# Kernel tuning notes

Hardware: AMD Instinct MI355X
Metric: run time of the kernel (lower is better)

Reference implementation:

```python
import jax, jax.numpy as jnp
import numpy as np

S, D, H, MLP = 2048, 1024, 16, 4096
DK = D // H
EPS = 1e-5  # torch LayerNorm default


def setup_inputs() -> dict:
    key = jax.random.key(0)
    ks = jax.random.split(key, 8)
    init = lambda k, shape, fan_in: jax.random.normal(k, shape, jnp.float32) * (fan_in ** -0.5)
    return {
        "x": jax.random.normal(ks[0], (S, D), jnp.float32),
        "wq": init(ks[1], (D, D), D), "bq": jnp.zeros((D,), jnp.float32),
        "wk": init(ks[2], (D, D), D), "bk": jnp.zeros((D,), jnp.float32),
        "wv": init(ks[3], (D, D), D), "bv": jnp.zeros((D,), jnp.float32),
        "wo": init(ks[4], (D, D), D), "bo": jnp.zeros((D,), jnp.float32),
        "w1": init(ks[5], (D, MLP), D), "b1": jnp.zeros((MLP,), jnp.float32),
        "w2": init(ks[6], (MLP, D), MLP), "b2": jnp.zeros((D,), jnp.float32),
        "ln1_g": jnp.ones((D,), jnp.float32), "ln1_b": jnp.zeros((D,), jnp.float32),
        "ln2_g": jnp.ones((D,), jnp.float32), "ln2_b": jnp.zeros((D,), jnp.float32),
    }


def _layernorm(x, g, b):
    m = jnp.mean(x, axis=-1, keepdims=True)
    v = jnp.var(x, axis=-1, keepdims=True)
    return (x - m) * jax.lax.rsqrt(v + EPS) * g + b


def reference(x, wq, bq, wk, bk, wv, bv, wo, bo, w1, b1, w2, b2, ln1_g, ln1_b, ln2_g, ln2_b):
    # --- residual 1: pre-LN multi-head self-attention ---
    h = _layernorm(x, ln1_g, ln1_b)
    q = (h @ wq + bq).reshape(S, H, DK).transpose(1, 0, 2)  # [H,S,DK]
    k = (h @ wk + bk).reshape(S, H, DK).transpose(1, 0, 2)
    v = (h @ wv + bv).reshape(S, H, DK).transpose(1, 0, 2)
    scores = jnp.einsum('hqd,hkd->hqk', q, k) / jnp.sqrt(jnp.float32(DK))  # [H,S,S]
    attn = jax.nn.softmax(scores, axis=-1)
    o = jnp.einsum('hqk,hkd->hqd', attn, v)  # [H,S,DK]
    # Faithful to original: x.contiguous().view(S, -1) is a raw reshape of the
    # [H,S,DK] buffer (no transpose back to [S,H,DK]).
    o = o.reshape(S, D)
    x = x + (o @ wo + bo)
    # --- residual 2: pre-LN GELU FFN ---
    h2 = _layernorm(x, ln2_g, ln2_b)
    f = jax.nn.gelu(h2 @ w1 + b1, approximate=False)  # torch nn.GELU = exact erf
    x = x + (f @ w2 + b2)
    return x
```

## Files before the change

### kernel.cpp

```cpp
#include <hip/hip_runtime.h>


constexpr int kS = 2048, kD = 1024, kH = 16, kDK = 64, kMLP = 4096;
constexpr float kEps = 1e-5f;

using u16 = unsigned short;
using u32 = unsigned int;
typedef float f32x4 __attribute__((ext_vector_type(4)));
typedef short bf16x8 __attribute__((ext_vector_type(8)));

__device__ __forceinline__ u16 f2b(float f) {
  u32 u = __builtin_bit_cast(u32, f);
  return (u16)((u + 0x7fffu + ((u >> 16) & 1u)) >> 16);
}

typedef const __attribute__((address_space(1))) u32* gas1;
typedef __attribute__((address_space(3))) u32* las3;
__device__ __forceinline__ void async16(const void* g, void* l) {
  __builtin_amdgcn_global_load_lds((gas1)g, (las3)l, 16, 0, 0);
}

__global__ __launch_bounds__(256)
void ln_kernel(const float* __restrict__ x, const float* __restrict__ g,
               const float* __restrict__ b, u16* __restrict__ out) {
  __shared__ float red[8];
  const int row = blockIdx.x, tid = threadIdx.x;
  const float4 v = *(const float4*)(x + (size_t)row * kD + tid * 4);
  float s = v.x + v.y + v.z + v.w;
  float ss = v.x * v.x + v.y * v.y + v.z * v.z + v.w * v.w;
#pragma unroll
  for (int d = 1; d < 64; d <<= 1) { s += __shfl_xor(s, d); ss += __shfl_xor(ss, d); }
  if ((tid & 63) == 0) { red[tid >> 6] = s; red[4 + (tid >> 6)] = ss; }
  __syncthreads();
  const float m = (red[0] + red[1] + red[2] + red[3]) * (1.f / kD);
  const float var = (red[4] + red[5] + red[6] + red[7]) * (1.f / kD) - m * m;
  const float r = rsqrtf(var + kEps);
  const float4 gv = *(const float4*)(g + tid * 4);
  const float4 bv = *(const float4*)(b + tid * 4);
  ushort4 o;
  o.x = f2b((v.x - m) * r * gv.x + bv.x);
  o.y = f2b((v.y - m) * r * gv.y + bv.y);
  o.z = f2b((v.z - m) * r * gv.z + bv.z);
  o.w = f2b((v.w - m) * r * gv.w + bv.w);
  *(ushort4*)(out + (size_t)row * kD + tid * 4) = o;
}

__global__ __launch_bounds__(256)
void transpose_cvt(const float* __restrict__ in, u16* __restrict__ out, int R, int C) {
  __shared__ float tile[32][33];
  const int c0 = blockIdx.x * 32, r0 = blockIdx.y * 32;
  const int x = threadIdx.x, y = threadIdx.y;
#pragma unroll
  for (int i = 0; i < 4; ++i)
    tile[y + i * 8][x] = in[(size_t)(r0 + y + i * 8) * C + c0 + x];
  __syncthreads();
#pragma unroll
  for (int i = 0; i < 4; ++i)
    out[(size_t)(c0 + y + i * 8) * R + r0 + x] = f2b(tile[x][y + i * 8]);
}

__global__ void concat_bias(const float* __restrict__ bq, const float* __restrict__ bk,
                            const float* __restrict__ bv, float* __restrict__ out) {
  int i = blockIdx.x * 256 + threadIdx.x;
  out[i] = i < kD ? bq[i] : (i < 2 * kD ? bk[i - kD] : bv[i - 2 * kD]);
}

__global__ __launch_bounds__(256)
void vtrans(const u16* __restrict__ qkv, u16* __restrict__ vt) {
  __shared__ u16 t[64][72];
  const int s0 = blockIdx.x * 64, h = blockIdx.y, tid = threadIdx.x;
#pragma unroll
  for (int r = 0; r < 2; ++r) {
    int chunk = r * 256 + tid, row = chunk >> 3, col = (chunk & 7) * 8;
    uint4 v = *(const uint4*)(qkv + (size_t)(s0 + row) * 3072 + 2 * kD + h * 64 + col);
    *(uint4*)(&t[row][col]) = v;
  }
  __syncthreads();
#pragma unroll
  for (int r = 0; r < 2; ++r) {
    int chunk = r * 256 + tid, drow = chunk >> 3, scol = (chunk & 7) * 8;
    u16 tmp[8];
#pragma unroll
    for (int j = 0; j < 8; ++j) tmp[j] = t[scol + j][drow];
    *(uint4*)(vt + (size_t)h * 64 * kS + (size_t)drow * kS + s0 + scol) = *(uint4*)tmp;
  }
}

template <int EPI>
__global__ __launch_bounds__(256, 2)
void gemm_bt(const u16* __restrict__ A, const u16* __restrict__ Bt,
             const float* __restrict__ bias, void* __restrict__ Cout,
             int N, int K, int Ksub) {
  constexpr int BM = 128, BN = 128, BK = 32;
  constexpr int MT = 4, NT = 4;
  __shared__ u16 As[BM * BK];
  __shared__ u16 Bs[BN * BK];
  const int tid = threadIdx.x;
  const int w = tid >> 6, l = tid & 63;
  const int wm = w >> 1, wn = w & 1;
  const int row0 = blockIdx.y * BM, col0 = blockIdx.x * BN;
  const int koff = blockIdx.z * Ksub;

  const int sc = ((l & 3) ^ ((l >> 3) & 3)) * 8;
  const u16* Ag = A + (size_t)(row0 + w * 16 + (l >> 2)) * K + koff + sc;
  const u16* Bg = Bt + (size_t)(col0 + w * 16 + (l >> 2)) * K + koff + sc;
  u16* AsW = As + w * 512;
  u16* BsW = Bs + w * 512;

  f32x4 acc[MT][NT] = {};
  const int q = l >> 4;

  for (int kt = 0; kt < Ksub; kt += BK) {
#pragma unroll
    for (int r = 0; r < 2; ++r) async16(Ag + (size_t)r * 64 * K + kt, AsW + r * 2048);
#pragma unroll
    for (int r = 0; r < 2; ++r) async16(Bg + (size_t)r * 64 * K + kt, BsW + r * 2048);
    __syncthreads();
    bf16x8 af[MT], bfr[NT];
#pragma unroll
    for (int i = 0; i < MT; ++i) {
      const int ra = wm * 64 + i * 16 + (l & 15);
      af[i] = *(const bf16x8*)(As + ra * 32 + (q ^ ((ra >> 1) & 3)) * 8);
    }
#pragma unroll
    for (int j = 0; j < NT; ++j) {
      const int rb = wn * 64 + j * 16 + (l & 15);
      bfr[j] = *(const bf16x8*)(Bs + rb * 32 + (q ^ ((rb >> 1) & 3)) * 8);
    }
#pragma unroll
    for (int i = 0; i < MT; ++i)
#pragma unroll
      for (int j = 0; j < NT; ++j)
        acc[i][j] = __builtin_amdgcn_mfma_f32_16x16x32_bf16(af[i], bfr[j], acc[i][j], 0, 0, 0);
    __syncthreads();
  }

  float* Pf = nullptr;
  if constexpr (EPI == 3)
    Pf = (float*)Cout + (size_t)blockIdx.z * gridDim.y * BM * N;
#pragma unroll
  for (int i = 0; i < MT; ++i) {
    const int row = row0 + wm * 64 + i * 16 + ((l >> 4) << 2);
#pragma unroll
    for (int j = 0; j < NT; ++j) {
      const int col = col0 + wn * 64 + j * 16 + (l & 15);
      float bb = 0.f;
      if constexpr (EPI != 3) bb = bias[col];
#pragma unroll
      for (int r = 0; r < 4; ++r) {
        const size_t idx = (size_t)(row + r) * N + col;
        float v = acc[i][j][r] + bb;
        if constexpr (EPI == 0) {
          ((u16*)Cout)[idx] = f2b(v);
        } else if constexpr (EPI == 1) {
          ((u16*)Cout)[idx] = f2b(0.5f * v * (1.f + erff(v * 0.7071067811865475f)));
        } else {
          Pf[idx] = v;
        }
      }
    }
  }
}

template <int KS>
__global__ __launch_bounds__(256)
void reduce_add(const float* __restrict__ parts, const float* __restrict__ bias,
                const float* __restrict__ res, float* __restrict__ out,
                int N, size_t strideMN) {
  const size_t b = ((size_t)blockIdx.x * 256 + threadIdx.x) * 4;
  float4 a = *(const float4*)(res + b);
  const float4 bv = *(const float4*)(bias + (b & (size_t)(N - 1)));
  a.x += bv.x; a.y += bv.y; a.z += bv.z; a.w += bv.w;
#pragma unroll
  for (int s = 0; s < KS; ++s) {
    const float4 p = *(const float4*)(parts + s * strideMN + b);
    a.x += p.x; a.y += p.y; a.z += p.z; a.w += p.w;
  }
  *(float4*)(out + b) = a;
}

__global__ __launch_bounds__(256, 2)
void flash_attn(const u16* __restrict__ qkv, const u16* __restrict__ vt,
                u16* __restrict__ og) {
  constexpr int LQ = 72;
  constexpr int LV = 136;
  __shared__ u16 Qs[64 * LQ];
  __shared__ u16 Ks[128 * LQ];
  __shared__ u16 Vs[64 * LV];
  __shared__ u16 Ps[4][16 * LV];
  const int tid = threadIdx.x, w = tid >> 6, l = tid & 63;
  const int h = blockIdx.y, q0 = blockIdx.x * 64;

#pragma unroll
  for (int r = 0; r < 2; ++r) {
    int chunk = r * 256 + tid, row = chunk >> 3, col = (chunk & 7) * 8;
    uint4 v = *(const uint4*)(qkv + (size_t)(q0 + row) * 3072 + h * 64 + col);
    *(uint4*)(&Qs[row * LQ + col]) = v;
  }
  __syncthreads();
  bf16x8 qa[2];
#pragma unroll
  for (int kq = 0; kq < 2; ++kq)
    qa[kq] = *(const bf16x8*)(&Qs[(w * 16 + (l & 15)) * LQ + kq * 32 + (l >> 4) * 8]);

  f32x4 oacc[4] = {};
  float mi[4], li[4];
#pragma unroll
  for (int r = 0; r < 4; ++r) { mi[r] = -1e30f; li[r] = 0.f; }

  for (int kt = 0; kt < kS; kt += 128) {
    __syncthreads();
#pragma unroll
    for (int r = 0; r < 4; ++r) {
      int chunk = r * 256 + tid, row = chunk >> 3, col = (chunk & 7) * 8;
      uint4 v = *(const uint4*)(qkv + (size_t)(kt + row) * 3072 + kD + h * 64 + col);
      *(uint4*)(&Ks[row * LQ + col]) = v;
    }
#pragma unroll
    for (int r = 0; r < 4; ++r) {
      int chunk = r * 256 + tid, row = chunk >> 4, col = (chunk & 15) * 8;
      uint4 v = *(const uint4*)(vt + (size_t)h * 64 * kS + (size_t)row * kS + kt + col);
      *(uint4*)(&Vs[row * LV + col]) = v;
    }
    __syncthreads();

    f32x4 s[8];
#pragma unroll
    for (int n = 0; n < 8; ++n) {
      f32x4 z = {};
      bf16x8 kb0 = *(const bf16x8*)(&Ks[(n * 16 + (l & 15)) * LQ + (l >> 4) * 8]);
      bf16x8 kb1 = *(const bf16x8*)(&Ks[(n * 16 + (l & 15)) * LQ + 32 + (l >> 4) * 8]);
      z = __builtin_amdgcn_mfma_f32_16x16x32_bf16(qa[0], kb0, z, 0, 0, 0);
      z = __builtin_amdgcn_mfma_f32_16x16x32_bf16(qa[1], kb1, z, 0, 0, 0);
      s[n] = z;
    }
    float alpha[4];
#pragma unroll
    for (int r = 0; r < 4; ++r) {
      float m = -1e30f;
#pragma unroll
      for (int n = 0; n < 8; ++n) m = fmaxf(m, s[n][r]);
#pragma unroll
      for (int d = 1; d < 16; d <<= 1) m = fmaxf(m, __shfl_xor(m, d));
      m *= 0.125f;
      float mn = fmaxf(mi[r], m);
      alpha[r] = __expf(mi[r] - mn);
      mi[r] = mn;
      li[r] *= alpha[r];
    }
#pragma unroll
    for (int n = 0; n < 4; ++n)
#pragma unroll
      for (int r = 0; r < 4; ++r) oacc[n][r] *= alpha[r];
    float rs[4] = {0.f, 0.f, 0.f, 0.f};
#pragma unroll
    for (int n = 0; n < 8; ++n)
#pragma unroll
      for (int r = 0; r < 4; ++r) {
        float pv = __expf(s[n][r] * 0.125f - mi[r]);
        rs[r] += pv;
        Ps[w][((l >> 4) * 4 + r) * LV + n * 16 + (l & 15)] = f2b(pv);
      }
#pragma unroll
    for (int r = 0; r < 4; ++r) {
      float t = rs[r];
#pragma unroll
      for (int d = 1; d < 16; d <<= 1) t += __shfl_xor(t, d);
      li[r] += t;
    }
    bf16x8 pa[4];
#pragma unroll
    for (int ks = 0; ks < 4; ++ks)
      pa[ks] = *(const bf16x8*)(&Ps[w][(l & 15) * LV + ks * 32 + (l >> 4) * 8]);
#pragma unroll
    for (int n = 0; n < 4; ++n)
#pragma unroll
      for (int ks = 0; ks < 4; ++ks) {
        bf16x8 vb = *(const bf16x8*)(&Vs[(n * 16 + (l & 15)) * LV + ks * 32 + (l >> 4) * 8]);
        oacc[n] = __builtin_amdgcn_mfma_f32_16x16x32_bf16(pa[ks], vb, oacc[n], 0, 0, 0);
      }
  }
#pragma unroll
  for (int r = 0; r < 4; ++r) {
    float inv = 1.f / li[r];
    int srow = q0 + w * 16 + (l >> 4) * 4 + r;
#pragma unroll
    for (int n = 0; n < 4; ++n) {
      int d = n * 16 + (l & 15);
      og[(size_t)h * kS * kDK + (size_t)srow * kDK + d] = f2b(oacc[n][r] * inv);
    }
  }
}

extern "C" void kernel_launch(void* const* d_in, const int* in_sizes, int n_in,
                              void* d_out, int out_size, void* d_ws, size_t ws_size,
                              hipStream_t stream) {
  const float* x = (const float*)d_in[0];
  const float* wq = (const float*)d_in[1];
  const float* bq = (const float*)d_in[2];
  const float* wk = (const float*)d_in[3];
  const float* bk = (const float*)d_in[4];
  const float* wv = (const float*)d_in[5];
  const float* bv = (const float*)d_in[6];
  const float* wo = (const float*)d_in[7];
  const float* bo = (const float*)d_in[8];
  const float* w1 = (const float*)d_in[9];
  const float* b1 = (const float*)d_in[10];
  const float* w2 = (const float*)d_in[11];
  const float* b2 = (const float*)d_in[12];
  const float* ln1g = (const float*)d_in[13];
  const float* ln1b = (const float*)d_in[14];
  const float* ln2g = (const float*)d_in[15];
  const float* ln2b = (const float*)d_in[16];
  float* out = (float*)d_out;

  char* p = (char*)d_ws;
  auto alloc = [&](size_t bytes) { void* q = (void*)p; p += (bytes + 255) & ~(size_t)255; return q; };
  u16* h1 = (u16*)alloc((size_t)kS * kD * 2);
  u16* wqkvt = (u16*)alloc((size_t)3 * kD * kD * 2);
  u16* qkv = (u16*)alloc((size_t)kS * 3 * kD * 2);
  u16* vt = (u16*)alloc((size_t)kH * kDK * kS * 2);
  u16* og = (u16*)alloc((size_t)kS * kD * 2);
  u16* wot = (u16*)alloc((size_t)kD * kD * 2);
  u16* h2 = (u16*)alloc((size_t)kS * kD * 2);
  u16* w1t = (u16*)alloc((size_t)kD * kMLP * 2);
  float* bqkv = (float*)alloc((size_t)3 * kD * 4);
  float* x2 = (float*)alloc((size_t)kS * kD * 4);
  u16* fbuf = (u16*)alloc((size_t)kS * kMLP * 2);
  u16* w2t = (u16*)alloc((size_t)kMLP * kD * 2);
  float* part = (float*)d_ws;
  const size_t strideMN = (size_t)kS * kD;

  dim3 tb(32, 8);
  transpose_cvt<<<dim3(kD / 32, kD / 32), tb, 0, stream>>>(wq, wqkvt, kD, kD);
  transpose_cvt<<<dim3(kD / 32, kD / 32), tb, 0, stream>>>(wk, wqkvt + kD * kD, kD, kD);
  transpose_cvt<<<dim3(kD / 32, kD / 32), tb, 0, stream>>>(wv, wqkvt + 2 * kD * kD, kD, kD);
  transpose_cvt<<<dim3(kD / 32, kD / 32), tb, 0, stream>>>(wo, wot, kD, kD);
  transpose_cvt<<<dim3(kMLP / 32, kD / 32), tb, 0, stream>>>(w1, w1t, kD, kMLP);
  transpose_cvt<<<dim3(kD / 32, kMLP / 32), tb, 0, stream>>>(w2, w2t, kMLP, kD);
  concat_bias<<<dim3(12), dim3(256), 0, stream>>>(bq, bk, bv, bqkv);

  ln_kernel<<<dim3(kS), dim3(256), 0, stream>>>(x, ln1g, ln1b, h1);
  gemm_bt<0><<<dim3(3 * kD / 128, kS / 128, 1), dim3(256), 0, stream>>>(
      h1, wqkvt, bqkv, qkv, 3 * kD, kD, kD);
  vtrans<<<dim3(kS / 64, kH), dim3(256), 0, stream>>>(qkv, vt);
  flash_attn<<<dim3(kS / 64, kH), dim3(256), 0, stream>>>(qkv, vt, og);
  gemm_bt<3><<<dim3(kD / 128, kS / 128, 2), dim3(256), 0, stream>>>(
      og, wot, nullptr, part, kD, kD, kD / 2);
  reduce_add<2><<<dim3(kS * kD / 4 / 256), dim3(256), 0, stream>>>(
      part, bo, x, x2, kD, strideMN);
  ln_kernel<<<dim3(kS), dim3(256), 0, stream>>>(x2, ln2g, ln2b, h2);
  gemm_bt<1><<<dim3(kMLP / 128, kS / 128, 1), dim3(256), 0, stream>>>(
      h2, w1t, b1, fbuf, kMLP, kD, kD);
  gemm_bt<3><<<dim3(kD / 128, kS / 128, 4), dim3(256), 0, stream>>>(
      fbuf, w2t, nullptr, part, kD, kMLP, kMLP / 4);
  reduce_add<4><<<dim3(kS * kD / 4 / 256), dim3(256), 0, stream>>>(
      part, b2, x2, out, kD, strideMN);
}
```

Measured before the change: 321.5 us.

## Split flash attention over two KV halves with register prefetch and combine kernel

Flash attention now splits the key/value sequence into two halves on a third grid dimension. This doubles the block count so the CUs fill better. Each half writes unnormalized fp32 partial outputs plus the running max and sum, and a new combine kernel merges them into bf16. The kernel also prefetches the next K/V tile into registers while computing the current one, and reuses the Q staging buffer as the P scratch buffer to cut LDS so the launch-bounds occupancy target can rise to 3. In exchange it adds an extra launch and fp32 partial traffic, and the partials live in workspace space borrowed from x2 and fbuf.

Result: slower. 368.9 us (+14.7%).

```diff
diff --git a/kernel.cpp b/kernel.cpp
--- a/kernel.cpp
+++ b/kernel.cpp
@@ -179,60 +179,81 @@
   *(float4*)(out + b) = a;
 }
 
-__global__ __launch_bounds__(256, 2)
+__global__ __launch_bounds__(256, 3)
 void flash_attn(const u16* __restrict__ qkv, const u16* __restrict__ vt,
-                u16* __restrict__ og) {
+                float* __restrict__ Op, float* __restrict__ Ml) {
   constexpr int LQ = 72;
   constexpr int LV = 136;
-  __shared__ u16 Qs[64 * LQ];
+  constexpr int LP = 140;
+  __shared__ u16 PsQ[4 * 16 * LP];
   __shared__ u16 Ks[128 * LQ];
   __shared__ u16 Vs[64 * LV];
-  __shared__ u16 Ps[4][16 * LV];
   const int tid = threadIdx.x, w = tid >> 6, l = tid & 63;
-  const int h = blockIdx.y, q0 = blockIdx.x * 64;
+  const int h = blockIdx.y, q0 = blockIdx.x * 64, z = blockIdx.z;
+  const int kt0 = z * (kS / 2);
+
+  const u16* Kg = qkv + kD + h * 64;
+  const u16* Vg = vt + (size_t)h * 64 * kS;
+
+  uint4 kreg[4], vreg[4];
+  auto load_tile = [&](int kt) {
+#pragma unroll
+    for (int r = 0; r < 4; ++r) {
+      int c = r * 256 + tid;
+      kreg[r] = *(const uint4*)(Kg + (size_t)(kt + (c >> 3)) * 3072 + (c & 7) * 8);
+    }
+#pragma unroll
+    for (int r = 0; r < 4; ++r) {
+      int c = r * 256 + tid;
+      vreg[r] = *(const uint4*)(Vg + (size_t)(c >> 4) * kS + kt + (c & 15) * 8);
+    }
+  };
+  auto store_tile = [&]() {
+#pragma unroll
+    for (int r = 0; r < 4; ++r) {
+      int c = r * 256 + tid;
+      *(uint4*)(&Ks[(c >> 3) * LQ + (c & 7) * 8]) = kreg[r];
+    }
+#pragma unroll
+    for (int r = 0; r < 4; ++r) {
+      int c = r * 256 + tid;
+      *(uint4*)(&Vs[(c >> 4) * LV + (c & 15) * 8]) = vreg[r];
+    }
+  };
 
 #pragma unroll
   for (int r = 0; r < 2; ++r) {
-    int chunk = r * 256 + tid, row = chunk >> 3, col = (chunk & 7) * 8;
-    uint4 v = *(const uint4*)(qkv + (size_t)(q0 + row) * 3072 + h * 64 + col);
-    *(uint4*)(&Qs[row * LQ + col]) = v;
-  }
+    int c = r * 256 + tid;
+    uint4 v = *(const uint4*)(qkv + (size_t)(q0 + (c >> 3)) * 3072 + h * 64 + (c & 7) * 8);
+    *(uint4*)(&PsQ[(c >> 3) * LQ + (c & 7) * 8]) = v;
+  }
+  load_tile(kt0);
   __syncthreads();
   bf16x8 qa[2];
 #pragma unroll
   for (int kq = 0; kq < 2; ++kq)
-    qa[kq] = *(const bf16x8*)(&Qs[(w * 16 + (l & 15)) * LQ + kq * 32 + (l >> 4) * 8]);
+    qa[kq] = *(const bf16x8*)(&PsQ[(w * 16 + (l & 15)) * LQ + kq * 32 + (l >> 4) * 8]);
+  u16* Ps = PsQ + w * 16 * LP;
 
   f32x4 oacc[4] = {};
   float mi[4], li[4];
 #pragma unroll
   for (int r = 0; r < 4; ++r) { mi[r] = -1e30f; li[r] = 0.f; }
 
-  for (int kt = 0; kt < kS; kt += 128) {
+  for (int it = 0; it < 8; ++it) {
+    store_tile();
     __syncthreads();
-#pragma unroll
-    for (int r = 0; r < 4; ++r) {
-      int chunk = r * 256 + tid, row = chunk >> 3, col = (chunk & 7) * 8;
-      uint4 v = *(const uint4*)(qkv + (size_t)(kt + row) * 3072 + kD + h * 64 + col);
-      *(uint4*)(&Ks[row * LQ + col]) = v;
-    }
-#pragma unroll
-    for (int r = 0; r < 4; ++r) {
-      int chunk = r * 256 + tid, row = chunk >> 4, col = (chunk & 15) * 8;
-      uint4 v = *(const uint4*)(vt + (size_t)h * 64 * kS + (size_t)row * kS + kt + col);
-      *(uint4*)(&Vs[row * LV + col]) = v;
-    }
-    __syncthreads();
+    if (it < 7) load_tile(kt0 + (it + 1) * 128);
 
     f32x4 s[8];
 #pragma unroll
     for (int n = 0; n < 8; ++n) {
-      f32x4 z = {};
+      f32x4 zz = {};
       bf16x8 kb0 = *(const bf16x8*)(&Ks[(n * 16 + (l & 15)) * LQ + (l >> 4) * 8]);
       bf16x8 kb1 = *(const bf16x8*)(&Ks[(n * 16 + (l & 15)) * LQ + 32 + (l >> 4) * 8]);
-      z = __builtin_amdgcn_mfma_f32_16x16x32_bf16(qa[0], kb0, z, 0, 0, 0);
-      z = __builtin_amdgcn_mfma_f32_16x16x32_bf16(qa[1], kb1, z, 0, 0, 0);
-      s[n] = z;
+      zz = __builtin_amdgcn_mfma_f32_16x16x32_bf16(qa[0], kb0, zz, 0, 0, 0);
+      zz = __builtin_amdgcn_mfma_f32_16x16x32_bf16(qa[1], kb1, zz, 0, 0, 0);
+      s[n] = zz;
     }
     float alpha[4];
 #pragma unroll
@@ -259,7 +280,7 @@
       for (int r = 0; r < 4; ++r) {
         float pv = __expf(s[n][r] * 0.125f - mi[r]);
         rs[r] += pv;
-        Ps[w][((l >> 4) * 4 + r) * LV + n * 16 + (l & 15)] = f2b(pv);
+        Ps[((l >> 4) * 4 + r) * LP + n * 16 + (l & 15)] = f2b(pv);
       }
 #pragma unroll
     for (int r = 0; r < 4; ++r) {
@@ -271,7 +292,7 @@
     bf16x8 pa[4];
 #pragma unroll
     for (int ks = 0; ks < 4; ++ks)
-      pa[ks] = *(const bf16x8*)(&Ps[w][(l & 15) * LV + ks * 32 + (l >> 4) * 8]);
+      pa[ks] = *(const bf16x8*)(&Ps[(l & 15) * LP + ks * 32 + (l >> 4) * 8]);
 #pragma unroll
     for (int n = 0; n < 4; ++n)
 #pragma unroll
@@ -279,17 +300,41 @@
         bf16x8 vb = *(const bf16x8*)(&Vs[(n * 16 + (l & 15)) * LV + ks * 32 + (l >> 4) * 8]);
         oacc[n] = __builtin_amdgcn_mfma_f32_16x16x32_bf16(pa[ks], vb, oacc[n], 0, 0, 0);
       }
-  }
+    __syncthreads();
+  }
+
 #pragma unroll
   for (int r = 0; r < 4; ++r) {
-    float inv = 1.f / li[r];
-    int srow = q0 + w * 16 + (l >> 4) * 4 + r;
-#pragma unroll
-    for (int n = 0; n < 4; ++n) {
-      int d = n * 16 + (l & 15);
-      og[(size_t)h * kS * kDK + (size_t)srow * kDK + d] = f2b(oacc[n][r] * inv);
-    }
-  }
+    const int srow = q0 + w * 16 + (l >> 4) * 4 + r;
+    const size_t rowIdx = (size_t)(z * kH + h) * kS + srow;
+    if ((l & 15) == 0) { Ml[rowIdx * 2] = mi[r]; Ml[rowIdx * 2 + 1] = li[r]; }
+#pragma unroll
+    for (int n = 0; n < 4; ++n)
+      Op[rowIdx * kDK + n * 16 + (l & 15)] = oacc[n][r];
+  }
+}
+
+__global__ __launch_bounds__(256)
+void flash_combine(const float* __restrict__ Op, const float* __restrict__ Ml,
+                   u16* __restrict__ og) {
+  constexpr size_t HS = (size_t)kH * kS;
+  constexpr size_t ZO = HS * kDK;
+  const int t = blockIdx.x * 256 + threadIdx.x;
+  const int d4 = (t & 15) * 4;
+  const size_t row = (size_t)(t >> 4);
+  const float m0 = Ml[row * 2], l0 = Ml[row * 2 + 1];
+  const float m1 = Ml[(HS + row) * 2], l1 = Ml[(HS + row) * 2 + 1];
+  const float m = fmaxf(m0, m1);
+  const float w0 = __expf(m0 - m), w1 = __expf(m1 - m);
+  const float inv = 1.f / (w0 * l0 + w1 * l1);
+  const float4 a = *(const float4*)(Op + row * kDK + d4);
+  const float4 b = *(const float4*)(Op + ZO + row * kDK + d4);
+  ushort4 o;
+  o.x = f2b((w0 * a.x + w1 * b.x) * inv);
+  o.y = f2b((w0 * a.y + w1 * b.y) * inv);
+  o.z = f2b((w0 * a.z + w1 * b.z) * inv);
+  o.w = f2b((w0 * a.w + w1 * b.w) * inv);
+  *(ushort4*)(og + row * kDK + d4) = o;
 }
 
 extern "C" void kernel_launch(void* const* d_in, const int* in_sizes, int n_in,
@@ -329,6 +374,8 @@
   u16* fbuf = (u16*)alloc((size_t)kS * kMLP * 2);
   u16* w2t = (u16*)alloc((size_t)kMLP * kD * 2);
   float* part = (float*)d_ws;
+  float* Op = x2;
+  float* Ml = Op + (size_t)2 * kH * kS * kDK;
   const size_t strideMN = (size_t)kS * kD;
 
   dim3 tb(32, 8);
@@ -344,7 +391,8 @@
   gemm_bt<0><<<dim3(3 * kD / 128, kS / 128, 1), dim3(256), 0, stream>>>(
       h1, wqkvt, bqkv, qkv, 3 * kD, kD, kD);
   vtrans<<<dim3(kS / 64, kH), dim3(256), 0, stream>>>(qkv, vt);
-  flash_attn<<<dim3(kS / 64, kH), dim3(256), 0, stream>>>(qkv, vt, og);
+  flash_attn<<<dim3(kS / 64, kH, 2), dim3(256), 0, stream>>>(qkv, vt, Op, Ml);
+  flash_combine<<<dim3(kH * kS * 16 / 256), dim3(256), 0, stream>>>(Op, Ml, og);
   gemm_bt<3><<<dim3(kD / 128, kS / 128, 2), dim3(256), 0, stream>>>(
       og, wot, nullptr, part, kD, kD, kD / 2);
   reduce_add<2><<<dim3(kS * kD / 4 / 256), dim3(256), 0, stream>>>(
```
